# Optimization experiments

Measured on AMD Instinct MI355X. Metric: run time of the kernel, lower is better.

The kernel has to match this reference:

```python
import jax, jax.numpy as jnp
import numpy as np


def setup_inputs() -> dict:
    key = jax.random.key(0)
    k_y, k_cb = jax.random.split(key)
    B, C, H, W = 8, 192, 64, 64
    G, K = 8, 512
    d = C // G  # 24
    y = jax.random.normal(k_y, (B, C, H, W), dtype=jnp.float32)
    codebooks = jax.random.normal(k_cb, (G, K, d), dtype=jnp.float32)
    return {"y": y, "codebooks": codebooks}


def reference(y, codebooks):
    # y: [B, C, H, W]; codebooks: [G, K, d] with C == G*d
    B, C, H, W = y.shape
    G, K, d = codebooks.shape
    # split channels into G groups of dim d -> vectors at each spatial pos
    x = y.reshape(B, G, d, H, W).transpose(0, 3, 4, 1, 2)  # [B,H,W,G,d]
    x2 = jnp.sum(x * x, axis=-1, keepdims=True)            # [B,H,W,G,1]
    e2 = jnp.sum(codebooks * codebooks, axis=-1)           # [G,K]
    xe = jnp.einsum('bhwgd,gkd->bhwgk', x, codebooks)      # [B,H,W,G,K]
    dist = x2 - 2.0 * xe + e2                              # [B,H,W,G,K]
    idx = jnp.argmin(dist, axis=-1)                        # [B,H,W,G] int
    # gather quantized vectors per group (to_feather)
    q = codebooks[jnp.arange(G), idx]                      # [B,H,W,G,d]
    y_ba = q.transpose(0, 3, 4, 1, 2).reshape(B, C, H, W)  # [B,C,H,W]
    code_index = idx.transpose(0, 3, 1, 2)                 # [B,G,H,W]
    # straight-through estimator
    universal_ctx = y + jax.lax.stop_gradient(y_ba - y)
    return universal_ctx, y_ba, code_index[:, None]        # [B,1,G,H,W]
```

## Files before the change

### kernel.cpp

```cpp
#include <hip/hip_runtime.h>

#define B_   8
#define C_   192
#define HW_  4096
#define G_   8
#define K_   512
#define D_   24
#define CBSZ (K_ * D_)
#define THREADS 256

#define FRAG_HW   12288
#define IMG_HW    13312
#define LDS_BYTES 26624
#define TILES_PER_GROUP 2048
#define WAVES_PER_GROUP 768

typedef float  f32x4 __attribute__((ext_vector_type(4)));
typedef int    i32x4 __attribute__((ext_vector_type(4)));
typedef short  s16x8 __attribute__((ext_vector_type(8)));
typedef short  s16x4 __attribute__((ext_vector_type(4)));
typedef unsigned long long u64;

static __device__ __forceinline__ unsigned umin_(unsigned a, unsigned b){return a<b?a:b;}
static __device__ __forceinline__ unsigned umax_(unsigned a, unsigned b){return a>b?a:b;}
static __device__ __forceinline__ unsigned short f2bf(float x){
    unsigned u=__float_as_uint(x);
    return (unsigned short)((u + 0x7FFFu + ((u>>16)&1u))>>16);
}

__global__ __launch_bounds__(THREADS) void vq_stage(
    const float* __restrict__ cb, unsigned short* __restrict__ ws)
{
    const int g = blockIdx.x >> 3;
    const int s = blockIdx.x & 7;
    const int tid = threadIdx.x;
    const float* cbg = cb + g * CBSZ;
    unsigned short* img = ws + g * IMG_HW;

    for (int i = tid; i < 384; i += THREADS) {
        int gi = s * 384 + i;
        f32x4 v = ((const f32x4*)cbg)[gi];
        int i4 = gi << 2;
        int n  = i4 / 24;
        int k0 = i4 - n * 24;
        int off = (n >> 4) * 384 + (((k0 >> 3) << 4) + (n & 15)) * 8 + (k0 & 7);
        s16x4 h;
        h[0]=(short)f2bf(v[0]); h[1]=(short)f2bf(v[1]);
        h[2]=(short)f2bf(v[2]); h[3]=(short)f2bf(v[3]);
        *(s16x4*)(&img[off]) = h;
    }
    if (tid < 64) {
        int n = s * 64 + tid;
        const float* row = cbg + n * D_;
        double s0 = 0.0, s1 = 0.0;
        #pragma unroll
        for (int j = 0; j < D_; j += 2) {
            double v0 = (double)row[j], v1 = (double)row[j+1];
            s0 = fma(v0,v0,s0); s1 = fma(v1,v1,s1);
        }
        ((float*)(img + FRAG_HW))[n] = (float)(256.0 + s0 + s1);
    }
}

__global__ __launch_bounds__(THREADS, 6) void vq_mfma6(
    const float* __restrict__ y, const float* __restrict__ cb,
    const unsigned short* __restrict__ ws, float* __restrict__ out)
{
    __shared__ __align__(16) unsigned short sB[IMG_HW];

    const int bid = blockIdx.x;
    const int g = bid & 7;
    const int blkg = bid >> 3;
    const int tid = threadIdx.x;
    const int wave = tid >> 6, lane = tid & 63;
    const int c = lane & 15, q = lane >> 4;

    const float* cbg = cb + g * CBSZ;

    {
        const char* src = (const char*)(ws + g * IMG_HW);
        char* dst = (char*)sB;
        #pragma unroll
        for (int it = 0; it < 7; ++it) {
            int off = it * 4096 + tid * 16;
            if (off < LDS_BYTES)
                *(i32x4*)(dst + off) = *(const i32x4*)(src + off);
        }
    }
    __syncthreads();

    float* out0 = out;
    float* out1 = out + B_*C_*HW_;
    float* out2 = out + 2*B_*C_*HW_;

    const unsigned short* aptr = sB + (lane < 48 ? lane : lane - 48) * 8;
    const f32x4* e2p = (const f32x4*)((const float*)(sB + FRAG_HW) + (q << 2));

    const int wsid = (blkg << 2) + wave;

    for (int tt = wsid; tt < TILES_PER_GROUP; tt += WAVES_PER_GROUP) {
        const int bimg = tt >> 8;
        const int hw   = (tt & 255) << 4;
        const int ybase = (bimg*C_ + g*D_)*HW_ + hw;
        const float* yb = y + ybase;

        float xf[8];
        unsigned hx[4], lx[4];
        if (q < 3) {
            const float* yq = yb + (q*8)*HW_ + c;
            #pragma unroll
            for (int jj = 0; jj < 8; ++jj) xf[jj] = -2.0f * yq[jj*HW_];
            #pragma unroll
            for (int p2 = 0; p2 < 4; ++p2) {
                float f0 = xf[2*p2], f1 = xf[2*p2+1];
                unsigned u0 = __float_as_uint(f0), u1v = __float_as_uint(f1);
                hx[p2] = (u1v & 0xFFFF0000u) | (u0 >> 16);
                float l0 = f0 - __uint_as_float(u0 & 0xFFFF0000u);
                float l1 = f1 - __uint_as_float(u1v & 0xFFFF0000u);
                lx[p2] = (unsigned)f2bf(l0) | ((unsigned)f2bf(l1) << 16);
            }
        } else {
            #pragma unroll
            for (int jj = 0; jj < 8; ++jj) xf[jj] = 0.0f;
            hx[0]=0u; hx[1]=0u; hx[2]=0u; hx[3]=0u;
            lx[0]=0u; lx[1]=0u; lx[2]=0u; lx[3]=0u;
        }
        const s16x8 Xh = __builtin_bit_cast(s16x8, (i32x4){(int)hx[0],(int)hx[1],(int)hx[2],(int)hx[3]});
        const s16x8 Xl = __builtin_bit_cast(s16x8, (i32x4){(int)lx[0],(int)lx[1],(int)lx[2],(int)lx[3]});

        unsigned b1=0xFFFFFFFFu, b2=0xFFFFFFFFu, b3=0xFFFFFFFFu;
        const unsigned qr4 = (unsigned)(q << 2);
        #pragma unroll 8
        for (int t = 0; t < 32; ++t) {
            s16x8 eh = *(const s16x8*)(aptr + t * 384);
            f32x4 acc = e2p[t * 4];
            acc = __builtin_amdgcn_mfma_f32_16x16x32_bf16(eh, Xh, acc, 0,0,0);
            acc = __builtin_amdgcn_mfma_f32_16x16x32_bf16(eh, Xl, acc, 0,0,0);
            const unsigned cbase = ((unsigned)t << 4) + qr4;
            #pragma unroll
            for (int r = 0; r < 4; ++r) {
                unsigned key = (__float_as_uint(acc[r]) & 0xFFFFFE00u) + (cbase + r);
                unsigned t3, t2;
                asm("v_med3_u32 %0, %1, %2, %3" : "=v"(t3) : "v"(key), "v"(b2), "v"(b3));
                asm("v_med3_u32 %0, %1, %2, %3" : "=v"(t2) : "v"(key), "v"(b1), "v"(b2));
                b3 = t3; b2 = t2;
                b1 = umin_(b1, key);
            }
        }

        #pragma unroll
        for (int d = 16; d < 64; d <<= 1) {
            unsigned o1=__shfl_xor(b1,d,64), o2=__shfl_xor(b2,d,64), o3=__shfl_xor(b3,d,64);
            unsigned x = umax_(b1,o1);
            unsigned yv= umin_(b2,o2);
            unsigned w = umax_(b2,o2);
            unsigned z = umin_(b3,o3);
            b1 = umin_(b1,o1);
            b2 = umin_(x,yv);
            b3 = umin_(umax_(x,yv), umin_(w,z));
        }

        const float v1 = __uint_as_float(b1 & 0xFFFFFE00u);
        const float v2 = __uint_as_float(b2 & 0xFFFFFE00u);
        int kwin;
        if (__ballot((v2 - v1) < 0.20f) == 0ull) {
            kwin = (int)(b1 & 511u);
        } else {
            double xd[8];
            #pragma unroll
            for (int jj = 0; jj < 8; ++jj) xd[jj] = (double)xf[jj];
            const unsigned cands[3] = {b1, b2, b3};
            u64 bestk = ~0ull;
            #pragma unroll
            for (int ci = 0; ci < 3; ++ci) {
                int kc = (int)(cands[ci] & 511u);
                double s = 0.0;
                if (q < 3) {
                    const f32x4* ce4 = (const f32x4*)(cbg + kc*D_ + (q<<3));
                    float ef[8];
                    *(f32x4*)&ef[0] = ce4[0];
                    *(f32x4*)&ef[4] = ce4[1];
                    #pragma unroll
                    for (int jj = 0; jj < 8; ++jj) {
                        double ev = (double)ef[jj];
                        s = fma(ev, ev, s);
                        s = fma(xd[jj], ev, s);
                    }
                }
                s += __shfl_xor(s, 16, 64);
                s += __shfl_xor(s, 32, 64);
                s += 256.0;
                u64 kk = (((u64)__double_as_longlong(s)) & ~0x1FFull) | (u64)kc;
                bestk = kk < bestk ? kk : bestk;
            }
            kwin = (int)(bestk & 511ull);
        }

        const float* cw = cbg + kwin * D_;
        if (q < 3) {
            const f32x4* cw4 = (const f32x4*)(cw + (q<<3));
            float v[8];
            *(f32x4*)&v[0] = cw4[0];
            *(f32x4*)&v[4] = cw4[1];
            const int ob = ybase + (q*8)*HW_ + c;
            #pragma unroll
            for (int jj = 0; jj < 8; ++jj) {
                out0[ob + jj*HW_] = v[jj];
                out1[ob + jj*HW_] = v[jj];
            }
        }
        if (lane < 16)
            out2[(bimg*G_ + g)*HW_ + hw + lane] = (float)kwin;
    }
}

extern "C" void kernel_launch(void* const* d_in, const int* in_sizes, int n_in,
                              void* d_out, int out_size, void* d_ws, size_t ws_size,
                              hipStream_t stream) {
    const float* y  = (const float*)d_in[0];
    const float* cb = (const float*)d_in[1];
    float* out = (float*)d_out;
    unsigned short* ws = (unsigned short*)d_ws;

    vq_stage<<<dim3(64), dim3(THREADS), 0, stream>>>(cb, ws);
    const int nblocks = 192 * G_;
    vq_mfma6<<<dim3(nblocks), dim3(THREADS), 0, stream>>>(y, cb, ws, out);
}
```

Before: 114.0 us.

## Fuse codebook staging into main VQ kernel and widen blocks to 512 threads

Drops the separate codebook-staging kernel. Each block now converts its group's codebook to the bf16 fragment layout and computes the norms directly into LDS, which removes a kernel launch and the round trip through the workspace. Blocks grow to 512 threads (8 waves) and the grid becomes 1024 blocks, so each wave handles two tiles. In exchange, every block repeats the fp32-to-bf16 conversion and the double-precision norm computation, adding per-block prologue work.

```diff
diff --git a/kernel.cpp b/kernel.cpp
--- a/kernel.cpp
+++ b/kernel.cpp
@@ -7,13 +7,13 @@
 #define K_   512
 #define D_   24
 #define CBSZ (K_ * D_)
-#define THREADS 256
+#define THREADS 512
+#define NBLOCKS 1024
 
 #define FRAG_HW   12288
 #define IMG_HW    13312
-#define LDS_BYTES 26624
 #define TILES_PER_GROUP 2048
-#define WAVES_PER_GROUP 768
+#define WAVES_PER_GROUP 1024
 
 typedef float  f32x4 __attribute__((ext_vector_type(4)));
 typedef int    i32x4 __attribute__((ext_vector_type(4)));
@@ -28,17 +28,24 @@
     return (unsigned short)((u + 0x7FFFu + ((u>>16)&1u))>>16);
 }
 
-__global__ __launch_bounds__(THREADS) void vq_stage(
-    const float* __restrict__ cb, unsigned short* __restrict__ ws)
+__global__ __launch_bounds__(THREADS, 8) void vq_mfma7(
+    const float* __restrict__ y, const float* __restrict__ cb,
+    float* __restrict__ out)
 {
-    const int g = blockIdx.x >> 3;
-    const int s = blockIdx.x & 7;
+    __shared__ __align__(16) unsigned short sB[IMG_HW];
+
+    const int bid = blockIdx.x;
+    const int g = bid & 7;
+    const int blkg = bid >> 3;
     const int tid = threadIdx.x;
+    const int wave = tid >> 6, lane = tid & 63;
+    const int c = lane & 15, q = lane >> 4;
+
     const float* cbg = cb + g * CBSZ;
-    unsigned short* img = ws + g * IMG_HW;
-
-    for (int i = tid; i < 384; i += THREADS) {
-        int gi = s * 384 + i;
+
+    #pragma unroll
+    for (int it = 0; it < 6; ++it) {
+        int gi = it * THREADS + tid;
         f32x4 v = ((const f32x4*)cbg)[gi];
         int i4 = gi << 2;
         int n  = i4 / 24;
@@ -47,10 +54,10 @@
         s16x4 h;
         h[0]=(short)f2bf(v[0]); h[1]=(short)f2bf(v[1]);
         h[2]=(short)f2bf(v[2]); h[3]=(short)f2bf(v[3]);
-        *(s16x4*)(&img[off]) = h;
+        *(s16x4*)(&sB[off]) = h;
     }
-    if (tid < 64) {
-        int n = s * 64 + tid;
+    {
+        const int n = tid;
         const float* row = cbg + n * D_;
         double s0 = 0.0, s1 = 0.0;
         #pragma unroll
@@ -58,34 +65,7 @@
             double v0 = (double)row[j], v1 = (double)row[j+1];
             s0 = fma(v0,v0,s0); s1 = fma(v1,v1,s1);
         }
-        ((float*)(img + FRAG_HW))[n] = (float)(256.0 + s0 + s1);
-    }
-}
-
-__global__ __launch_bounds__(THREADS, 6) void vq_mfma6(
-    const float* __restrict__ y, const float* __restrict__ cb,
-    const unsigned short* __restrict__ ws, float* __restrict__ out)
-{
-    __shared__ __align__(16) unsigned short sB[IMG_HW];
-
-    const int bid = blockIdx.x;
-    const int g = bid & 7;
-    const int blkg = bid >> 3;
-    const int tid = threadIdx.x;
-    const int wave = tid >> 6, lane = tid & 63;
-    const int c = lane & 15, q = lane >> 4;
-
-    const float* cbg = cb + g * CBSZ;
-
-    {
-        const char* src = (const char*)(ws + g * IMG_HW);
-        char* dst = (char*)sB;
-        #pragma unroll
-        for (int it = 0; it < 7; ++it) {
-            int off = it * 4096 + tid * 16;
-            if (off < LDS_BYTES)
-                *(i32x4*)(dst + off) = *(const i32x4*)(src + off);
-        }
+        ((float*)(sB + FRAG_HW))[n] = (float)(256.0 + s0 + s1);
     }
     __syncthreads();
 
@@ -96,7 +76,7 @@
     const unsigned short* aptr = sB + (lane < 48 ? lane : lane - 48) * 8;
     const f32x4* e2p = (const f32x4*)((const float*)(sB + FRAG_HW) + (q << 2));
 
-    const int wsid = (blkg << 2) + wave;
+    const int wsid = (blkg << 3) + wave;
 
     for (int tt = wsid; tt < TILES_PER_GROUP; tt += WAVES_PER_GROUP) {
         const int bimg = tt >> 8;
@@ -220,9 +200,7 @@
     const float* y  = (const float*)d_in[0];
     const float* cb = (const float*)d_in[1];
     float* out = (float*)d_out;
-    unsigned short* ws = (unsigned short*)d_ws;
-
-    vq_stage<<<dim3(64), dim3(THREADS), 0, stream>>>(cb, ws);
-    const int nblocks = 192 * G_;
-    vq_mfma6<<<dim3(nblocks), dim3(THREADS), 0, stream>>>(y, cb, ws, out);
+    (void)d_ws; (void)ws_size;
+
+    vq_mfma7<<<dim3(NBLOCKS), dim3(THREADS), 0, stream>>>(y, cb, out);
 }
```

After: 112.7 us. About the same (-1.2%).
